# Kernel optimization log

Measured on AMD Instinct MI355X. Metric: run time of the kernel, lower is better.

## Reference

```python
import jax, jax.numpy as jnp
import numpy as np

B, C, H, W = 16, 256, 96, 96
PLANES = 64            # inplanes * ratio = 256 * 0.25
HEADS = 4
EPS = 1e-5             # BatchNorm eps


def setup_inputs() -> dict:
    key = jax.random.key(0)
    ks = jax.random.split(key, 8)
    HW = H * W
    G = HW // HEADS    # group size of the grouped 1x1 conv over spatial-positions-as-channels
    return {
        "x": jax.random.normal(ks[0], (B, C, H, W), jnp.float32),
        # input_conv: Conv1x1(C->PLANES) -> BN -> ReLU -> Conv1x1(PLANES->C)
        "w1": jax.random.normal(ks[1], (PLANES, C), jnp.float32) * (1.0 / np.sqrt(C)),
        "b1": jax.random.normal(ks[2], (PLANES,), jnp.float32) * 0.01,
        "gamma": jnp.ones((PLANES,), jnp.float32),
        "beta": jnp.zeros((PLANES,), jnp.float32),
        "mean": jnp.zeros((PLANES,), jnp.float32),
        "var": jnp.ones((PLANES,), jnp.float32),
        "w2": jax.random.normal(ks[3], (C, PLANES), jnp.float32) * (1.0 / np.sqrt(PLANES)),
        "b2": jax.random.normal(ks[4], (C,), jnp.float32) * 0.01,
        # conv_mask: Conv2d(HW, HEADS, k=1, groups=HEADS) -> weight [HEADS, G], bias [HEADS]
        "wm": jax.random.normal(ks[5], (HEADS, G), jnp.float32) * (1.0 / np.sqrt(G)),
        "bm": jax.random.normal(ks[6], (HEADS,), jnp.float32) * 0.01,
    }


def reference(x, w1, b1, gamma, beta, mean, var, w2, b2, wm, bm):
    Bx, Cx, Hx, Wx = x.shape
    G = (Hx * Wx) // HEADS
    # ---- input_conv: 1x1 conv -> BN (inference) -> ReLU -> 1x1 conv ----
    h = jnp.einsum('bchw,pc->bphw', x, w1) + b1[None, :, None, None]
    scale = (gamma / jnp.sqrt(var + EPS))[None, :, None, None]
    h = jax.nn.relu((h - mean[None, :, None, None]) * scale + beta[None, :, None, None])
    y = jnp.einsum('bphw,cp->bchw', h, w2) + b2[None, :, None, None]
    # ---- treat spatial positions as channels: [B, HEADS, G, C] ----
    ix = y.transpose(0, 2, 3, 1).reshape(Bx, HEADS, G, Cx)
    # grouped 1x1 conv over HW-channels -> logits [B, HEADS, C]
    logits = jnp.einsum('bhgc,hg->bhc', ix, wm) + bm[None, :, None]
    # softmax over channel axis (torch dim=2 of [B, HEADS, C, 1])
    mask = jax.nn.softmax(logits, axis=2)
    # context pooling matmul: [B,HEADS,G,C] @ [B,HEADS,C,1] -> [B,HEADS,G]
    ctx = jnp.einsum('bhgc,bhc->bhg', ix, mask)
    context = ctx.reshape(Bx, 1, Hx, Wx)
    # fusion_types = ('channel_add',)
    return x + context
```

## Files before the change

### kernel.cpp

```cpp
#include <hip/hip_runtime.h>

#define Bn 16
#define Cn 256
#define HWn 9216
#define Pn 64
#define HEADSn 4
#define Gn 2304
#define STILE 64
#define TILES_PER_B (HWn / STILE)
#define NBLK (Bn * TILES_PER_B)

typedef float f32x4 __attribute__((ext_vector_type(4)));
typedef short short8 __attribute__((ext_vector_type(8)));

static __device__ __forceinline__ unsigned short f2bf(float f) {
    unsigned int b = __builtin_bit_cast(unsigned int, f);
    unsigned int r = b + 0x7FFFu + ((b >> 16) & 1u);
    return (unsigned short)(r >> 16);
}

static __device__ __forceinline__ void gload_lds16(const void* g, void* l) {
    __builtin_amdgcn_global_load_lds((const __attribute__((address_space(1))) void*)g,
                                     (__attribute__((address_space(3))) void*)l, 16, 0, 0);
}

__global__ __launch_bounds__(256)
void k0_prep(const float* __restrict__ w1, const float* __restrict__ b1,
             const float* __restrict__ gamma, const float* __restrict__ beta,
             const float* __restrict__ mean, const float* __restrict__ var,
             float* __restrict__ scbc, short* __restrict__ w1s)
{
    const int gid = blockIdx.x * 256 + threadIdx.x;
    if (gid < 2048) {
        const int row = gid >> 5;
        const int kc  = (gid & 31) << 3;
        const float* p = w1 + row * Cn + kc;
        short8 v;
        #pragma unroll
        for (int j = 0; j < 8; ++j) v[j] = (short)f2bf(p[j]);
        const int idx = (row * Cn + kc) ^ ((row & 7) << 3);
        *reinterpret_cast<short8*>(&w1s[idx]) = v;
    }
    if (gid < Pn) {
        float s = gamma[gid] * rsqrtf(var[gid] + 1e-5f);
        scbc[gid] = s;
        scbc[Pn + gid] = (b1[gid] - mean[gid]) * s + beta[gid];
    }
}

template <int MODE>
__global__ __launch_bounds__(256, 2)
void gemm_pass(const float* __restrict__ x, const short* __restrict__ w1s,
               const float* __restrict__ scbc, const float* __restrict__ wm,
               float* __restrict__ hmp,
               const float* __restrict__ wmix, const float* __restrict__ bmix,
               float* __restrict__ out)
{
    __shared__ short w1l[Pn * Cn];
    __shared__ short xl[Cn * STILE];
    __shared__ float ctxl[STILE];
    __shared__ float hml[Pn];

    const int bid  = blockIdx.x;
    const int b    = bid / TILES_PER_B;
    const int tile = bid % TILES_PER_B;
    const int s0   = tile * STILE;
    const int head = s0 / Gn;
    const int t    = threadIdx.x;
    const int lane = t & 63;
    const int wv   = t >> 6;
    const int g    = lane >> 4;
    const int m16  = lane & 15;

    #pragma unroll
    for (int i = 0; i < 8; ++i) {
        const int chunk = i * 4 + wv;
        gload_lds16(w1s + chunk * 512 + lane * 8, &w1l[chunk * 512]);
    }

    const int c0 = t >> 3;
    const int s8 = t & 7;
    const float* xb = x + (size_t)b * Cn * HWn + s0 + s8 * 8;
    f32x4 xa[16];
    #pragma unroll
    for (int i = 0; i < 8; ++i) {
        const float* p = xb + (size_t)(c0 + 32 * i) * HWn;
        xa[2 * i]     = *reinterpret_cast<const f32x4*>(p);
        xa[2 * i + 1] = *reinterpret_cast<const f32x4*>(p + 4);
    }
    #pragma unroll
    for (int i = 0; i < 8; ++i) {
        const int c = c0 + 32 * i;
        short8 v;
        #pragma unroll
        for (int j = 0; j < 4; ++j) { v[j] = (short)f2bf(xa[2 * i][j]); v[4 + j] = (short)f2bf(xa[2 * i + 1][j]); }
        const int f   = (c & 7) ^ ((c >> 3) & 3);
        const int idx = (c * STILE + s8 * 8) ^ (f << 3);
        *reinterpret_cast<short8*>(&xl[idx]) = v;
    }
    if (MODE == 0 && t < Pn) hml[t] = 0.f;
    __syncthreads();

    f32x4 acc[4] = { {0,0,0,0}, {0,0,0,0}, {0,0,0,0}, {0,0,0,0} };
    const int sbase = wv * 16 + m16;
    #pragma unroll
    for (int ks = 0; ks < 8; ++ks) {
        short8 bf;
        #pragma unroll
        for (int j = 0; j < 8; ++j) {
            const int k = ks * 32 + g * 8 + j;
            bf[j] = xl[(k * STILE + sbase) ^ ((j ^ g) << 3)];
        }
        #pragma unroll
        for (int rt = 0; rt < 4; ++rt) {
            const int row = rt * 16 + m16;
            const int idx = (row * Cn + ks * 32 + g * 8) ^ ((row & 7) << 3);
            const short8 af = *reinterpret_cast<const short8*>(&w1l[idx]);
            acc[rt] = __builtin_amdgcn_mfma_f32_16x16x32_bf16(af, bf, acc[rt], 0, 0, 0);
        }
    }

    f32x4 xr[16];
    if (MODE == 1) {
        #pragma unroll
        for (int i = 0; i < 8; ++i) {
            const float* p = xb + (size_t)(c0 + 32 * i) * HWn;
            xr[2 * i]     = *reinterpret_cast<const f32x4*>(p);
            xr[2 * i + 1] = *reinterpret_cast<const f32x4*>(p + 4);
        }
    }

    float h[4][4];
    #pragma unroll
    for (int rt = 0; rt < 4; ++rt) {
        #pragma unroll
        for (int r = 0; r < 4; ++r) {
            const int p = rt * 16 + g * 4 + r;
            const float hv = acc[rt][r] * scbc[p] + scbc[Pn + p];
            h[rt][r] = hv > 0.f ? hv : 0.f;
        }
    }

    if (MODE == 0) {
        const float wmv = wm[s0 + sbase];
        #pragma unroll
        for (int rt = 0; rt < 4; ++rt) {
            #pragma unroll
            for (int r = 0; r < 4; ++r) {
                float v = h[rt][r] * wmv;
                v += __shfl_xor(v, 1); v += __shfl_xor(v, 2);
                v += __shfl_xor(v, 4); v += __shfl_xor(v, 8);
                if (m16 == 0) atomicAdd(&hml[rt * 16 + g * 4 + r], v);
            }
        }
        __syncthreads();
        if (t < Pn) hmp[bid * Pn + t] = hml[t];
    } else {
        const int bh = b * HEADSn + head;
        const float* wmx = wmix + bh * Pn;
        float cp = 0.f;
        #pragma unroll
        for (int rt = 0; rt < 4; ++rt) {
            #pragma unroll
            for (int r = 0; r < 4; ++r)
                cp = fmaf(wmx[rt * 16 + g * 4 + r], h[rt][r], cp);
        }
        cp += __shfl_xor(cp, 16);
        cp += __shfl_xor(cp, 32);
        if (lane < 16) ctxl[sbase] = cp + bmix[bh];
        __syncthreads();

        const f32x4 cv0 = *reinterpret_cast<const f32x4*>(&ctxl[s8 * 8]);
        const f32x4 cv1 = *reinterpret_cast<const f32x4*>(&ctxl[s8 * 8 + 4]);
        float* ob = out + (size_t)b * Cn * HWn + s0 + s8 * 8;
        #pragma unroll
        for (int i = 0; i < 8; ++i) {
            float* p = ob + (size_t)(c0 + 32 * i) * HWn;
            *reinterpret_cast<f32x4*>(p)     = xr[2 * i] + cv0;
            *reinterpret_cast<f32x4*>(p + 4) = xr[2 * i + 1] + cv1;
        }
    }
}

__global__ __launch_bounds__(256)
void k2_mask(const float* __restrict__ hmp, const float* __restrict__ w2,
             const float* __restrict__ b2, const float* __restrict__ wm,
             float* __restrict__ wmix, float* __restrict__ bmix)
{
    __shared__ float hms[Pn];
    __shared__ float masks[Cn];
    __shared__ float red[4];
    __shared__ float part[4][Pn];

    const int bh = blockIdx.x;
    const int head = bh & (HEADSn - 1);
    const int t = threadIdx.x;
    const int l = t & 63;
    const int wv = t >> 6;

    {
        const int p = t & 63, q = t >> 6;
        const float* base = hmp + ((size_t)(bh >> 2) * TILES_PER_B + (bh & 3) * 36) * Pn;
        float sp = 0.f;
        #pragma unroll
        for (int j = 0; j < 9; ++j) sp += base[(q + 4 * j) * Pn + p];
        part[q][p] = sp;
    }
    __syncthreads();
    if (t < Pn) hms[t] = part[0][t] + part[1][t] + part[2][t] + part[3][t];
    __syncthreads();

    float wsum = 0.f;
    for (int i = t; i < Gn; i += 256) wsum += wm[head * Gn + i];
    #pragma unroll
    for (int d = 1; d < 64; d <<= 1) wsum += __shfl_xor(wsum, d);
    if (l == 0) red[wv] = wsum;
    __syncthreads();
    wsum = red[0] + red[1] + red[2] + red[3];

    float lg = 0.f;
    #pragma unroll
    for (int k = 0; k < Pn; ++k) lg = fmaf(w2[t * Pn + k], hms[k], lg);
    lg = fmaf(b2[t], wsum, lg);

    float mx = lg;
    #pragma unroll
    for (int d = 1; d < 64; d <<= 1) mx = fmaxf(mx, __shfl_xor(mx, d));
    __syncthreads();
    if (l == 0) red[wv] = mx;
    __syncthreads();
    mx = fmaxf(fmaxf(red[0], red[1]), fmaxf(red[2], red[3]));
    const float ev = __expf(lg - mx);
    float sm = ev;
    #pragma unroll
    for (int d = 1; d < 64; d <<= 1) sm += __shfl_xor(sm, d);
    __syncthreads();
    if (l == 0) red[wv] = sm;
    __syncthreads();
    sm = red[0] + red[1] + red[2] + red[3];
    masks[t] = ev / sm;
    __syncthreads();

    {
        const int k = t & (Pn - 1);
        const int q = t >> 6;
        float wp = 0.f;
        #pragma unroll
        for (int i = 0; i < 64; ++i) {
            const int c = q * 64 + i;
            wp = fmaf(masks[c], w2[c * Pn + k], wp);
        }
        part[q][k] = wp;
    }
    __syncthreads();
    if (t < Pn) wmix[bh * Pn + t] = part[0][t] + part[1][t] + part[2][t] + part[3][t];

    float bp = masks[t] * b2[t];
    #pragma unroll
    for (int d = 1; d < 64; d <<= 1) bp += __shfl_xor(bp, d);
    __syncthreads();
    if (l == 0) red[wv] = bp;
    __syncthreads();
    if (t == 0) bmix[bh] = red[0] + red[1] + red[2] + red[3];
}

extern "C" void kernel_launch(void* const* d_in, const int* in_sizes, int n_in,
                              void* d_out, int out_size, void* d_ws, size_t ws_size,
                              hipStream_t stream)
{
    (void)in_sizes; (void)n_in; (void)out_size; (void)ws_size;
    const float* x     = (const float*)d_in[0];
    const float* w1    = (const float*)d_in[1];
    const float* b1    = (const float*)d_in[2];
    const float* gamma = (const float*)d_in[3];
    const float* beta  = (const float*)d_in[4];
    const float* mean  = (const float*)d_in[5];
    const float* var   = (const float*)d_in[6];
    const float* w2    = (const float*)d_in[7];
    const float* b2    = (const float*)d_in[8];
    const float* wm    = (const float*)d_in[9];

    float* out  = (float*)d_out;
    float* wsf  = (float*)d_ws;
    float* hmp  = wsf;
    float* wmix = hmp + NBLK * Pn;
    float* bmix = wmix + Bn * HEADSn * Pn;
    float* scbc = bmix + 64;
    short* w1s  = (short*)(scbc + 128);

    k0_prep<<<dim3(8), dim3(256), 0, stream>>>(w1, b1, gamma, beta, mean, var, scbc, w1s);
    gemm_pass<0><<<dim3(NBLK), dim3(256), 0, stream>>>(x, w1s, scbc, wm, hmp, nullptr, nullptr, nullptr);
    k2_mask<<<dim3(Bn * HEADSn), dim3(256), 0, stream>>>(hmp, w2, b2, wm, wmix, bmix);
    gemm_pass<1><<<dim3(NBLK), dim3(256), 0, stream>>>(x, w1s, scbc, wm, nullptr, wmix, bmix, out);
}
```

Before: 122.7 us.

## Materialize hidden activations in bf16 and replace second GEMM pass with streaming kernel

The first GEMM pass now writes the post-ReLU hidden activations (64 channels per position) to a bf16 workspace buffer. The final pass no longer reloads the w1 tile, re-converts x to bf16 or recomputes the MFMA GEMM. It reads the stored activations, does a 64-element dot product per position, and streams x+context to the output. This trades the recomputation for about 19 MB of extra global write and read traffic. The x load pattern also changes to 16-byte per-thread loads across 16 channel strides, and the occupancy hint is dropped.

```diff
diff --git a/kernel.cpp b/kernel.cpp
--- a/kernel.cpp
+++ b/kernel.cpp
@@ -11,6 +11,7 @@
 #define NBLK (Bn * TILES_PER_B)
 
 typedef float f32x4 __attribute__((ext_vector_type(4)));
+typedef short short4v __attribute__((ext_vector_type(4)));
 typedef short short8 __attribute__((ext_vector_type(8)));
 
 static __device__ __forceinline__ unsigned short f2bf(float f) {
@@ -18,7 +19,10 @@
     unsigned int r = b + 0x7FFFu + ((b >> 16) & 1u);
     return (unsigned short)(r >> 16);
 }
-
+static __device__ __forceinline__ float bf2f(unsigned short u) {
+    unsigned int b = ((unsigned int)u) << 16;
+    return __builtin_bit_cast(float, b);
+}
 static __device__ __forceinline__ void gload_lds16(const void* g, void* l) {
     __builtin_amdgcn_global_load_lds((const __attribute__((address_space(1))) void*)g,
                                      (__attribute__((address_space(3))) void*)l, 16, 0, 0);
@@ -48,220 +52,244 @@
     }
 }
 
-template <int MODE>
-__global__ __launch_bounds__(256, 2)
-void gemm_pass(const float* __restrict__ x, const short* __restrict__ w1s,
-               const float* __restrict__ scbc, const float* __restrict__ wm,
-               float* __restrict__ hmp,
+__global__ __launch_bounds__(256)
+void k1_gemm(const float* __restrict__ x, const short* __restrict__ w1s,
+             const float* __restrict__ scbc, const float* __restrict__ wm,
+             float* __restrict__ hmp, short* __restrict__ hg)
+{
+    __shared__ short w1l[Pn * Cn];
+    __shared__ short xl[Cn * STILE];
+    __shared__ float hml[Pn];
+
+    const int bid  = blockIdx.x;
+    const int b    = bid / TILES_PER_B;
+    const int tile = bid % TILES_PER_B;
+    const int s0   = tile * STILE;
+    const int t    = threadIdx.x;
+    const int lane = t & 63;
+    const int wv   = t >> 6;
+    const int g    = lane >> 4;
+    const int m16  = lane & 15;
+    const int sbase = wv * 16 + m16;
+
+    #pragma unroll
+    for (int i = 0; i < 8; ++i) {
+        const int chunk = i * 4 + wv;
+        gload_lds16(w1s + chunk * 512 + lane * 8, &w1l[chunk * 512]);
+    }
+
+    const int c0 = t >> 4;
+    const int s4 = t & 15;
+    const float* xb = x + (size_t)b * Cn * HWn + s0 + s4 * 4;
+    f32x4 xa[16];
+    #pragma unroll
+    for (int i = 0; i < 16; ++i)
+        xa[i] = *reinterpret_cast<const f32x4*>(xb + (size_t)(c0 + 16 * i) * HWn);
+
+    if (t < Pn) hml[t] = 0.f;
+
+    #pragma unroll
+    for (int i = 0; i < 16; ++i) {
+        const int c = c0 + 16 * i;
+        short4v v;
+        #pragma unroll
+        for (int j = 0; j < 4; ++j) v[j] = (short)f2bf(xa[i][j]);
+        const int f   = (c & 7) ^ ((c >> 3) & 3);
+        const int idx = (c * STILE + s4 * 4) ^ (f << 3);
+        *reinterpret_cast<short4v*>(&xl[idx]) = v;
+    }
+    __syncthreads();
+
+    f32x4 acc[4] = { {0,0,0,0}, {0,0,0,0}, {0,0,0,0}, {0,0,0,0} };
+    #pragma unroll
+    for (int ks = 0; ks < 8; ++ks) {
+        short8 bf;
+        #pragma unroll
+        for (int j = 0; j < 8; ++j) {
+            const int k = ks * 32 + g * 8 + j;
+            bf[j] = xl[(k * STILE + sbase) ^ ((j ^ g) << 3)];
+        }
+        #pragma unroll
+        for (int rt = 0; rt < 4; ++rt) {
+            const int row = rt * 16 + m16;
+            const int idx = (row * Cn + ks * 32 + g * 8) ^ ((row & 7) << 3);
+            const short8 af = *reinterpret_cast<const short8*>(&w1l[idx]);
+            acc[rt] = __builtin_amdgcn_mfma_f32_16x16x32_bf16(af, bf, acc[rt], 0, 0, 0);
+        }
+    }
+
+    float h[4][4];
+    #pragma unroll
+    for (int rt = 0; rt < 4; ++rt) {
+        #pragma unroll
+        for (int r = 0; r < 4; ++r) {
+            const int p = rt * 16 + g * 4 + r;
+            const float hv = acc[rt][r] * scbc[p] + scbc[Pn + p];
+            h[rt][r] = hv > 0.f ? hv : 0.f;
+        }
+    }
+
+    const float wmv = wm[s0 + sbase];
+    #pragma unroll
+    for (int rt = 0; rt < 4; ++rt) {
+        #pragma unroll
+        for (int r = 0; r < 4; ++r) {
+            float v = h[rt][r] * wmv;
+            v += __shfl_xor(v, 1); v += __shfl_xor(v, 2);
+            v += __shfl_xor(v, 4); v += __shfl_xor(v, 8);
+            if (m16 == 0) atomicAdd(&hml[rt * 16 + g * 4 + r], v);
+        }
+    }
+    __syncthreads();
+
+    short* ht = xl;
+    #pragma unroll
+    for (int rt = 0; rt < 4; ++rt) {
+        short4v hv;
+        #pragma unroll
+        for (int r = 0; r < 4; ++r) hv[r] = (short)f2bf(h[rt][r]);
+        *reinterpret_cast<short4v*>(&ht[sbase * 72 + rt * 16 + g * 4]) = hv;
+    }
+    __syncthreads();
+
+    {
+        const int s = t >> 2, q = t & 3;
+        const short8 a0 = *reinterpret_cast<const short8*>(&ht[s * 72 + q * 16]);
+        const short8 a1 = *reinterpret_cast<const short8*>(&ht[s * 72 + q * 16 + 8]);
+        short* dst = hg + ((size_t)b * HWn + s0 + s) * Pn + q * 16;
+        *reinterpret_cast<short8*>(dst)     = a0;
+        *reinterpret_cast<short8*>(dst + 8) = a1;
+    }
+    if (t < Pn) hmp[bid * Pn + t] = hml[t];
+}
+
+__global__ __launch_bounds__(256)
+void k2_mask(const float* __restrict__ hmp, const float* __restrict__ w2,
+             const float* __restrict__ b2, const float* __restrict__ wm,
+             float* __restrict__ wmix, float* __restrict__ bmix)
+{
+    __shared__ float hms[Pn];
+    __shared__ float masks[Cn];
+    __shared__ float red[4];
+    __shared__ float part[4][Pn];
+
+    const int bh = blockIdx.x;
+    const int head = bh & (HEADSn - 1);
+    const int t = threadIdx.x;
+    const int l = t & 63;
+    const int wv = t >> 6;
+
+    {
+        const int p = t & 63, q = t >> 6;
+        const float* base = hmp + ((size_t)(bh >> 2) * TILES_PER_B + (bh & 3) * 36) * Pn;
+        float sp = 0.f;
+        #pragma unroll
+        for (int j = 0; j < 9; ++j) sp += base[(q + 4 * j) * Pn + p];
+        part[q][p] = sp;
+    }
+    __syncthreads();
+    if (t < Pn) hms[t] = part[0][t] + part[1][t] + part[2][t] + part[3][t];
+    __syncthreads();
+
+    float wsum = 0.f;
+    for (int i = t; i < Gn; i += 256) wsum += wm[head * Gn + i];
+    #pragma unroll
+    for (int d = 1; d < 64; d <<= 1) wsum += __shfl_xor(wsum, d);
+    if (l == 0) red[wv] = wsum;
+    __syncthreads();
+    wsum = red[0] + red[1] + red[2] + red[3];
+
+    float lg = 0.f;
+    #pragma unroll
+    for (int k = 0; k < Pn; ++k) lg = fmaf(w2[t * Pn + k], hms[k], lg);
+    lg = fmaf(b2[t], wsum, lg);
+
+    float mx = lg;
+    #pragma unroll
+    for (int d = 1; d < 64; d <<= 1) mx = fmaxf(mx, __shfl_xor(mx, d));
+    __syncthreads();
+    if (l == 0) red[wv] = mx;
+    __syncthreads();
+    mx = fmaxf(fmaxf(red[0], red[1]), fmaxf(red[2], red[3]));
+    const float ev = __expf(lg - mx);
+    float sm = ev;
+    #pragma unroll
+    for (int d = 1; d < 64; d <<= 1) sm += __shfl_xor(sm, d);
+    __syncthreads();
+    if (l == 0) red[wv] = sm;
+    __syncthreads();
+    sm = red[0] + red[1] + red[2] + red[3];
+    masks[t] = ev / sm;
+    __syncthreads();
+
+    {
+        const int k = t & (Pn - 1);
+        const int q = t >> 6;
+        float wp = 0.f;
+        #pragma unroll
+        for (int i = 0; i < 64; ++i) {
+            const int c = q * 64 + i;
+            wp = fmaf(masks[c], w2[c * Pn + k], wp);
+        }
+        part[q][k] = wp;
+    }
+    __syncthreads();
+    if (t < Pn) wmix[bh * Pn + t] = part[0][t] + part[1][t] + part[2][t] + part[3][t];
+
+    float bp = masks[t] * b2[t];
+    #pragma unroll
+    for (int d = 1; d < 64; d <<= 1) bp += __shfl_xor(bp, d);
+    __syncthreads();
+    if (l == 0) red[wv] = bp;
+    __syncthreads();
+    if (t == 0) bmix[bh] = red[0] + red[1] + red[2] + red[3];
+}
+
+__global__ __launch_bounds__(256)
+void k3_stream(const float* __restrict__ x, const short* __restrict__ hg,
                const float* __restrict__ wmix, const float* __restrict__ bmix,
                float* __restrict__ out)
 {
-    __shared__ short w1l[Pn * Cn];
-    __shared__ short xl[Cn * STILE];
     __shared__ float ctxl[STILE];
-    __shared__ float hml[Pn];
 
     const int bid  = blockIdx.x;
     const int b    = bid / TILES_PER_B;
     const int tile = bid % TILES_PER_B;
     const int s0   = tile * STILE;
     const int head = s0 / Gn;
+    const int bh   = b * HEADSn + head;
     const int t    = threadIdx.x;
-    const int lane = t & 63;
-    const int wv   = t >> 6;
-    const int g    = lane >> 4;
-    const int m16  = lane & 15;
-
-    #pragma unroll
-    for (int i = 0; i < 8; ++i) {
-        const int chunk = i * 4 + wv;
-        gload_lds16(w1s + chunk * 512 + lane * 8, &w1l[chunk * 512]);
-    }
-
-    const int c0 = t >> 3;
-    const int s8 = t & 7;
-    const float* xb = x + (size_t)b * Cn * HWn + s0 + s8 * 8;
-    f32x4 xa[16];
-    #pragma unroll
-    for (int i = 0; i < 8; ++i) {
-        const float* p = xb + (size_t)(c0 + 32 * i) * HWn;
-        xa[2 * i]     = *reinterpret_cast<const f32x4*>(p);
-        xa[2 * i + 1] = *reinterpret_cast<const f32x4*>(p + 4);
-    }
-    #pragma unroll
-    for (int i = 0; i < 8; ++i) {
-        const int c = c0 + 32 * i;
-        short8 v;
-        #pragma unroll
-        for (int j = 0; j < 4; ++j) { v[j] = (short)f2bf(xa[2 * i][j]); v[4 + j] = (short)f2bf(xa[2 * i + 1][j]); }
-        const int f   = (c & 7) ^ ((c >> 3) & 3);
-        const int idx = (c * STILE + s8 * 8) ^ (f << 3);
-        *reinterpret_cast<short8*>(&xl[idx]) = v;
-    }
-    if (MODE == 0 && t < Pn) hml[t] = 0.f;
-    __syncthreads();
-
-    f32x4 acc[4] = { {0,0,0,0}, {0,0,0,0}, {0,0,0,0}, {0,0,0,0} };
-    const int sbase = wv * 16 + m16;
-    #pragma unroll
-    for (int ks = 0; ks < 8; ++ks) {
-        short8 bf;
-        #pragma unroll
-        for (int j = 0; j < 8; ++j) {
-            const int k = ks * 32 + g * 8 + j;
-            bf[j] = xl[(k * STILE + sbase) ^ ((j ^ g) << 3)];
-        }
-        #pragma unroll
-        for (int rt = 0; rt < 4; ++rt) {
-            const int row = rt * 16 + m16;
-            const int idx = (row * Cn + ks * 32 + g * 8) ^ ((row & 7) << 3);
-            const short8 af = *reinterpret_cast<const short8*>(&w1l[idx]);
-            acc[rt] = __builtin_amdgcn_mfma_f32_16x16x32_bf16(af, bf, acc[rt], 0, 0, 0);
-        }
-    }
-
-    f32x4 xr[16];
-    if (MODE == 1) {
+
+    if (t < STILE) {
+        const short* hr = hg + ((size_t)b * HWn + s0 + t) * Pn;
+        const float* wmx = wmix + bh * Pn;
+        float acc = 0.f;
         #pragma unroll
         for (int i = 0; i < 8; ++i) {
-            const float* p = xb + (size_t)(c0 + 32 * i) * HWn;
-            xr[2 * i]     = *reinterpret_cast<const f32x4*>(p);
-            xr[2 * i + 1] = *reinterpret_cast<const f32x4*>(p + 4);
-        }
-    }
-
-    float h[4][4];
-    #pragma unroll
-    for (int rt = 0; rt < 4; ++rt) {
-        #pragma unroll
-        for (int r = 0; r < 4; ++r) {
-            const int p = rt * 16 + g * 4 + r;
-            const float hv = acc[rt][r] * scbc[p] + scbc[Pn + p];
-            h[rt][r] = hv > 0.f ? hv : 0.f;
-        }
-    }
-
-    if (MODE == 0) {
-        const float wmv = wm[s0 + sbase];
-        #pragma unroll
-        for (int rt = 0; rt < 4; ++rt) {
+            const short8 v = *reinterpret_cast<const short8*>(hr + i * 8);
+            const f32x4 w0 = *reinterpret_cast<const f32x4*>(wmx + i * 8);
+            const f32x4 w1v = *reinterpret_cast<const f32x4*>(wmx + i * 8 + 4);
             #pragma unroll
-            for (int r = 0; r < 4; ++r) {
-                float v = h[rt][r] * wmv;
-                v += __shfl_xor(v, 1); v += __shfl_xor(v, 2);
-                v += __shfl_xor(v, 4); v += __shfl_xor(v, 8);
-                if (m16 == 0) atomicAdd(&hml[rt * 16 + g * 4 + r], v);
+            for (int j = 0; j < 4; ++j) {
+                acc = fmaf(bf2f((unsigned short)v[j]), w0[j], acc);
+                acc = fmaf(bf2f((unsigned short)v[4 + j]), w1v[j], acc);
             }
         }
-        __syncthreads();
-        if (t < Pn) hmp[bid * Pn + t] = hml[t];
-    } else {
-        const int bh = b * HEADSn + head;
-        const float* wmx = wmix + bh * Pn;
-        float cp = 0.f;
-        #pragma unroll
-        for (int rt = 0; rt < 4; ++rt) {
-            #pragma unroll
-            for (int r = 0; r < 4; ++r)
-                cp = fmaf(wmx[rt * 16 + g * 4 + r], h[rt][r], cp);
-        }
-        cp += __shfl_xor(cp, 16);
-        cp += __shfl_xor(cp, 32);
-        if (lane < 16) ctxl[sbase] = cp + bmix[bh];
-        __syncthreads();
-
-        const f32x4 cv0 = *reinterpret_cast<const f32x4*>(&ctxl[s8 * 8]);
-        const f32x4 cv1 = *reinterpret_cast<const f32x4*>(&ctxl[s8 * 8 + 4]);
-        float* ob = out + (size_t)b * Cn * HWn + s0 + s8 * 8;
-        #pragma unroll
-        for (int i = 0; i < 8; ++i) {
-            float* p = ob + (size_t)(c0 + 32 * i) * HWn;
-            *reinterpret_cast<f32x4*>(p)     = xr[2 * i] + cv0;
-            *reinterpret_cast<f32x4*>(p + 4) = xr[2 * i + 1] + cv1;
-        }
-    }
-}
-
-__global__ __launch_bounds__(256)
-void k2_mask(const float* __restrict__ hmp, const float* __restrict__ w2,
-             const float* __restrict__ b2, const float* __restrict__ wm,
-             float* __restrict__ wmix, float* __restrict__ bmix)
-{
-    __shared__ float hms[Pn];
-    __shared__ float masks[Cn];
-    __shared__ float red[4];
-    __shared__ float part[4][Pn];
-
-    const int bh = blockIdx.x;
-    const int head = bh & (HEADSn - 1);
-    const int t = threadIdx.x;
-    const int l = t & 63;
-    const int wv = t >> 6;
-
-    {
-        const int p = t & 63, q = t >> 6;
-        const float* base = hmp + ((size_t)(bh >> 2) * TILES_PER_B + (bh & 3) * 36) * Pn;
-        float sp = 0.f;
-        #pragma unroll
-        for (int j = 0; j < 9; ++j) sp += base[(q + 4 * j) * Pn + p];
-        part[q][p] = sp;
-    }
-    __syncthreads();
-    if (t < Pn) hms[t] = part[0][t] + part[1][t] + part[2][t] + part[3][t];
-    __syncthreads();
-
-    float wsum = 0.f;
-    for (int i = t; i < Gn; i += 256) wsum += wm[head * Gn + i];
-    #pragma unroll
-    for (int d = 1; d < 64; d <<= 1) wsum += __shfl_xor(wsum, d);
-    if (l == 0) red[wv] = wsum;
-    __syncthreads();
-    wsum = red[0] + red[1] + red[2] + red[3];
-
-    float lg = 0.f;
-    #pragma unroll
-    for (int k = 0; k < Pn; ++k) lg = fmaf(w2[t * Pn + k], hms[k], lg);
-    lg = fmaf(b2[t], wsum, lg);
-
-    float mx = lg;
-    #pragma unroll
-    for (int d = 1; d < 64; d <<= 1) mx = fmaxf(mx, __shfl_xor(mx, d));
-    __syncthreads();
-    if (l == 0) red[wv] = mx;
-    __syncthreads();
-    mx = fmaxf(fmaxf(red[0], red[1]), fmaxf(red[2], red[3]));
-    const float ev = __expf(lg - mx);
-    float sm = ev;
-    #pragma unroll
-    for (int d = 1; d < 64; d <<= 1) sm += __shfl_xor(sm, d);
-    __syncthreads();
-    if (l == 0) red[wv] = sm;
-    __syncthreads();
-    sm = red[0] + red[1] + red[2] + red[3];
-    masks[t] = ev / sm;
-    __syncthreads();
-
-    {
-        const int k = t & (Pn - 1);
-        const int q = t >> 6;
-        float wp = 0.f;
-        #pragma unroll
-        for (int i = 0; i < 64; ++i) {
-            const int c = q * 64 + i;
-            wp = fmaf(masks[c], w2[c * Pn + k], wp);
-        }
-        part[q][k] = wp;
-    }
-    __syncthreads();
-    if (t < Pn) wmix[bh * Pn + t] = part[0][t] + part[1][t] + part[2][t] + part[3][t];
-
-    float bp = masks[t] * b2[t];
-    #pragma unroll
-    for (int d = 1; d < 64; d <<= 1) bp += __shfl_xor(bp, d);
-    __syncthreads();
-    if (l == 0) red[wv] = bp;
-    __syncthreads();
-    if (t == 0) bmix[bh] = red[0] + red[1] + red[2] + red[3];
+        ctxl[t] = acc + bmix[bh];
+    }
+    __syncthreads();
+
+    const int c0 = t >> 4;
+    const int s4 = t & 15;
+    const f32x4 cv = *reinterpret_cast<const f32x4*>(&ctxl[s4 * 4]);
+    const float* xb = x + (size_t)b * Cn * HWn + s0 + s4 * 4;
+    float* ob = out + (size_t)b * Cn * HWn + s0 + s4 * 4;
+    #pragma unroll
+    for (int i = 0; i < 16; ++i) {
+        const size_t off = (size_t)(c0 + 16 * i) * HWn;
+        *reinterpret_cast<f32x4*>(ob + off) =
+            *reinterpret_cast<const f32x4*>(xb + off) + cv;
+    }
 }
 
 extern "C" void kernel_launch(void* const* d_in, const int* in_sizes, int n_in,
@@ -287,9 +315,10 @@
     float* bmix = wmix + Bn * HEADSn * Pn;
     float* scbc = bmix + 64;
     short* w1s  = (short*)(scbc + 128);
+    short* hg   = w1s + Pn * Cn;
 
     k0_prep<<<dim3(8), dim3(256), 0, stream>>>(w1, b1, gamma, beta, mean, var, scbc, w1s);
-    gemm_pass<0><<<dim3(NBLK), dim3(256), 0, stream>>>(x, w1s, scbc, wm, hmp, nullptr, nullptr, nullptr);
+    k1_gemm<<<dim3(NBLK), dim3(256), 0, stream>>>(x, w1s, scbc, wm, hmp, hg);
     k2_mask<<<dim3(Bn * HEADSn), dim3(256), 0, stream>>>(hmp, w2, b2, wm, wmix, bmix);
-    gemm_pass<1><<<dim3(NBLK), dim3(256), 0, stream>>>(x, w1s, scbc, wm, nullptr, wmix, bmix, out);
-}
+    k3_stream<<<dim3(NBLK), dim3(256), 0, stream>>>(x, hg, wmix, bmix, out);
+}
```

Result: faster. 107.9 us (-12.0%).
